# Optimization experiments

Measured on AMD Instinct MI355X. Metric: run time of the kernel, lower is better.

The kernel has to match this reference:

```python
import jax, jax.numpy as jnp
import numpy as np

# ---------------- irreps metadata: list of (mul, l, parity) ----------------
IR_A  = [(1, 0, 1)]                                        # '0e' input scalars
IR_B  = [(10,0,1),(10,0,-1),(10,0,1),(5,1,1),(5,1,-1)]     # Gate input, dim 60
IR_C  = [(10,0,1),(10,0,-1),(5,1,1),(5,1,-1)]              # Gate output, dim 50
IR_D  = [(1,0,-1),(6,0,1)]                                 # '0o + 6x0e', dim 7
IR_SH = [(1,0,1),(1,1,-1)]                                 # '0e + 1o'
CONVS = [(IR_A,IR_B),(IR_C,IR_B),(IR_C,IR_B),(IR_C,IR_B),(IR_C,IR_D)]
R_BASIS  = 2
DIAMETER = 5.0   # source used 1.5 -> degenerate 1^3 kernel; enlarged to exercise the steerable conv
STEP     = 1.0

def irdim(ir):
    return sum(m*(2*l+1) for m,l,_ in ir)

def irslices(ir):
    out, o = [], 0
    for m,l,_ in ir:
        d = m*(2*l+1); out.append(slice(o,o+d)); o += d
    return out

# normalized Clebsch-Gordan (wigner3j * sqrt(2*l_out+1)) for l<=1
_eps = np.zeros((3,3,3))
for a,b,c in [(0,1,2),(1,2,0),(2,0,1)]:
    _eps[a,b,c] = 1.0; _eps[b,a,c] = -1.0
CG = {
    (0,0,0): np.ones((1,1,1)),
    (0,1,1): np.eye(3).reshape(1,3,3),
    (1,0,1): np.eye(3).reshape(3,1,3),
    (1,1,0): (np.eye(3)/np.sqrt(3.0)).reshape(3,3,1),
    (1,1,1): _eps/np.sqrt(2.0),
}

def tp_ins(ir1, iro):
    ins = []
    for i1,(m1,l1,p1) in enumerate(ir1):
        for i2,(m2,l2,p2) in enumerate(IR_SH):
            for io,(mo,lo,po) in enumerate(iro):
                if po == p1*p2 and abs(l1-l2) <= lo <= l1+l2:
                    ins.append((i1,i2,io))
    return ins

def tp_numel(ir1, iro):
    return sum(R_BASIS*ir1[i1][0]*IR_SH[i2][0]*iro[io][0] for i1,i2,io in tp_ins(ir1,iro))

def lin_ins(ir1, iro):
    return [(i,j) for i,(m1,l1,p1) in enumerate(ir1)
                  for j,(m2,l2,p2) in enumerate(iro) if l1==l2 and p1==p2]

def lin_numel(ir1, iro):
    return sum(ir1[i][0]*iro[j][0] for i,j in lin_ins(ir1,iro))

def _lattice_features():
    # lattice offsets, smooth_finite radial basis (with cutoff) and SH ('0e+1o', component norm)
    r = DIAMETER/2.0
    s = int(np.floor(r/STEP))
    c = np.arange(-s, s+1, dtype=np.float64)*STEP
    lat = np.stack(np.meshgrid(c, c, c, indexing='ij'), -1)            # [K,K,K,3]
    d = np.linalg.norm(lat, axis=-1)
    vals = np.linspace(0.0, r, R_BASIS+2)[1:-1]
    step = vals[1]-vals[0]
    diff = (d[...,None]-vals)/step
    sus = lambda t: np.where(t>0, np.exp(-1.0/np.where(t>0, t, 1.0)), 0.0)
    emb = 1.14136*np.exp(2.0)*sus(diff+1.0)*sus(1.0-diff)              # [K,K,K,R]
    unit = lat/np.maximum(d, 1e-9)[...,None]
    sh = np.concatenate([np.ones_like(d)[...,None],
                         np.sqrt(3.0)*unit[...,[1,2,0]]], -1)          # [K,K,K,4], e3nn (y,z,x) order
    return jnp.asarray(emb, jnp.float32), jnp.asarray(sh, jnp.float32)

EMB, SH = _lattice_features()

def build_kernel(ir_in, ir_out, tw, lw):
    sin, sout, ssh = irslices(ir_in), irslices(ir_out), irslices(IR_SH)
    K = EMB.shape[0]
    k = jnp.zeros((K, K, K, irdim(ir_in), irdim(ir_out)), jnp.float32)
    off = 0
    for i1,i2,io in tp_ins(ir_in, ir_out):
        m1,l1,_ = ir_in[i1]; m2,l2,_ = IR_SH[i2]; mo,lo,_ = ir_out[io]
        n = R_BASIS*m1*m2*mo
        w = tw[off:off+n].reshape(R_BASIS, m1, mo); off += n           # m2 == 1 for SH
        cg = jnp.asarray(CG[(l1,l2,lo)], jnp.float32)
        alpha = 1.0/np.sqrt(m1*m2*R_BASIS)
        shseg = SH[..., ssh[i2]]                                       # [K,K,K,2l2+1]
        blk = alpha*jnp.einsum('xyzr,ruw,xyzj,ijk->xyzuiwk', EMB, w, shseg, cg)
        k = k.at[:,:,:, sin[i1], sout[io]].add(
            blk.reshape(K, K, K, m1*(2*l1+1), mo*(2*lo+1)))
    # self-connection Linear at the kernel center (radial basis vanishes at r=0)
    M = jnp.zeros((irdim(ir_in), irdim(ir_out)), jnp.float32)
    off = 0
    for i,j in lin_ins(ir_in, ir_out):
        m1,l1,_ = ir_in[i]; mo,_,_ = ir_out[j]
        w = lw[off:off+m1*mo].reshape(m1, mo); off += m1*mo
        eye = jnp.eye(2*l1+1, dtype=jnp.float32)
        blk = (1.0/np.sqrt(m1))*jnp.einsum('uw,ik->uiwk', w, eye)
        M = M.at[sin[i], sout[j]].add(blk.reshape(m1*(2*l1+1), mo*(2*l1+1)))
    cc = K//2
    return k.at[cc, cc, cc].set(M)

def equiv_conv(x, k):
    return jax.lax.conv_general_dilated(x, k, (1,1,1), 'SAME',
        dimension_numbers=('NXYZC', 'XYZIO', 'NXYZC'))

def gate(y):
    # Gate('10x0e+10x0o', [gelu, tanh], '10x0e', [sigmoid], '5x1e+5x1o')
    s = jnp.concatenate([jax.nn.gelu(y[..., :10]), jnp.tanh(y[..., 10:20])], -1)
    g = jax.nn.sigmoid(y[..., 20:30])                                  # 10 gate scalars
    v = y[..., 30:60].reshape(y.shape[:-1]+(10,3))*g[..., None]        # gate 5x1e + 5x1o
    return jnp.concatenate([s, v.reshape(y.shape[:-1]+(30,))], -1)

def _forward(x, tws, lws):
    y = x
    for i,(a,b) in enumerate(CONVS):
        y = equiv_conv(y, build_kernel(a, b, tws[i], lws[i]))
        if i < len(CONVS)-1:
            y = gate(y)
    return jnp.sum(y, axis=(1, 2, 3))                                  # [B, 7]

def setup_inputs() -> dict:
    key = jax.random.key(0)
    ks = jax.random.split(key, 11)
    inp = {'x': jax.random.normal(ks[0], (2, 48, 48, 48, 1), jnp.float32)}
    for i,(a,b) in enumerate(CONVS):
        inp[f'tp_w{i}'] = jax.random.normal(ks[1+i], (tp_numel(a,b),), jnp.float32)
        inp[f'lin_w{i}'] = jax.random.normal(ks[6+i], (lin_numel(a,b),), jnp.float32)
    return inp

def reference(x, tp_w0, tp_w1, tp_w2, tp_w3, tp_w4,
              lin_w0, lin_w1, lin_w2, lin_w3, lin_w4):
    return _forward(x, [tp_w0, tp_w1, tp_w2, tp_w3, tp_w4],
                    [lin_w0, lin_w1, lin_w2, lin_w3, lin_w4])
```

## Files before the change

### kernel.cpp

```cpp
#include <hip/hip_runtime.h>
#include <hip/hip_bf16.h>
#include <math.h>


typedef __attribute__((ext_vector_type(8))) short bf16x8;
typedef __attribute__((ext_vector_type(4))) float f32x4;
typedef __attribute__((ext_vector_type(4))) unsigned int u32x4;

struct TpPath { int off, ci, co, m1, l1, i2, mo, lo; float alpha; };
struct LinPath { int off, ci, co, m1, l, mo; float norm; };

__device__ __constant__ TpPath g_tp[19] = {
  {0,  0,  0, 1, 0, 0, 10, 0, 0.70710678f},
  {20, 0, 20, 1, 0, 0, 10, 0, 0.70710678f},
  {40, 0, 45, 1, 0, 1,  5, 1, 0.70710678f},
  {0,    0,  0, 10, 0, 0, 10, 0, 0.22360680f},
  {200,  0, 20, 10, 0, 0, 10, 0, 0.22360680f},
  {400,  0, 45, 10, 0, 1,  5, 1, 0.22360680f},
  {500, 10, 10, 10, 0, 0, 10, 0, 0.22360680f},
  {700, 10, 30, 10, 0, 1,  5, 1, 0.22360680f},
  {800, 20, 30,  5, 1, 0,  5, 1, 0.31622777f},
  {850, 20, 10,  5, 1, 1, 10, 0, 0.31622777f},
  {950, 20, 45,  5, 1, 1,  5, 1, 0.31622777f},
  {1000,35, 45,  5, 1, 0,  5, 1, 0.31622777f},
  {1050,35,  0,  5, 1, 1, 10, 0, 0.31622777f},
  {1150,35, 20,  5, 1, 1, 10, 0, 0.31622777f},
  {1250,35, 30,  5, 1, 1,  5, 1, 0.31622777f},
  {0,    0, 1, 10, 0, 0, 6, 0, 0.22360680f},
  {120, 10, 0, 10, 0, 0, 1, 0, 0.22360680f},
  {140, 20, 0,  5, 1, 1, 1, 0, 0.31622777f},
  {150, 35, 1,  5, 1, 1, 6, 0, 0.31622777f},
};

__device__ __constant__ LinPath g_lin[9] = {
  {0,  0,  0, 1, 0, 10, 1.0f},
  {10, 0, 20, 1, 0, 10, 1.0f},
  {0,   0,  0, 10, 0, 10, 0.31622777f},
  {100, 0, 20, 10, 0, 10, 0.31622777f},
  {200,10, 10, 10, 0, 10, 0.31622777f},
  {300,20, 30,  5, 1,  5, 0.44721360f},
  {325,35, 45,  5, 1,  5, 0.44721360f},
  {0,  0, 1, 10, 0, 6, 0.31622777f},
  {60,10, 0, 10, 0, 1, 0.31622777f},
};

__device__ inline float sus_f(float t) { return t > 0.f ? __expf(-1.f / t) : 0.f; }

__global__ void build_tp_kernel(const float* __restrict__ tw, float* __restrict__ kbuf,
                                int CIN, int COUT, int path_base) {
  TpPath p = g_tp[path_base + blockIdx.x];
  const int dl1 = 2 * p.l1 + 1, dlo = 2 * p.lo + 1;
  const int du = p.m1 * dl1, dw = p.mo * dlo;
  const int total = 125 * du * dw;
  const float C0 = 1.14136f * expf(2.0f);
  for (int e = threadIdx.x; e < total; e += blockDim.x) {
    int xyz = e / (du * dw);
    int rem = e % (du * dw);
    int ui = rem / dw, wk = rem % dw;
    int u = ui / dl1, i = ui % dl1;
    int w = wk / dlo, kk = wk % dlo;
    int kx = xyz / 25, ky = (xyz / 5) % 5, kz = xyz % 5;
    float cx = (float)(kx - 2), cy = (float)(ky - 2), cz = (float)(kz - 2);
    float d = sqrtf(cx * cx + cy * cy + cz * cz);
    float t = 1.2f * d;
    float e0 = C0 * sus_f(t) * sus_f(2.f - t);
    float e1 = C0 * sus_f(t - 1.f) * sus_f(3.f - t);
    float radial = e0 * tw[p.off + (0 * p.m1 + u) * p.mo + w] +
                   e1 * tw[p.off + (1 * p.m1 + u) * p.mo + w];
    float invd = (d > 0.f) ? 1.f / d : 0.f;
    const float s3 = 1.7320508f;
    float sh1[3] = { s3 * cy * invd, s3 * cz * invd, s3 * cx * invd };
    float shfac;
    if (p.l1 == 0 && p.i2 == 0)      shfac = 1.f;
    else if (p.l1 == 0)              shfac = sh1[kk];
    else if (p.i2 == 0)              shfac = (i == kk) ? 1.f : 0.f;
    else if (p.lo == 0)              shfac = sh1[i] * 0.57735027f;
    else {
      if (i == kk) shfac = 0.f;
      else {
        int j = 3 - i - kk;
        float sgn = (j == (i + 1) % 3) ? 1.f : -1.f;
        shfac = sgn * sh1[j] * 0.70710678f;
      }
    }
    kbuf[(size_t)(xyz * CIN + p.ci + ui) * COUT + p.co + wk] = p.alpha * radial * shfac;
  }
}

__global__ void set_center_kernel(const float* __restrict__ lw, float* __restrict__ kbuf,
                                  int CIN, int COUT, int lin_base, int nlin) {
  for (int l = 0; l < nlin; l++) {
    LinPath q = g_lin[lin_base + l];
    int dl = 2 * q.l + 1;
    int tot = q.m1 * q.mo * dl;
    for (int e = threadIdx.x; e < tot; e += blockDim.x) {
      int u = e / (q.mo * dl);
      int r = e % (q.mo * dl);
      int w = r / dl, ii = r % dl;
      kbuf[(size_t)(62 * CIN + q.ci + u * dl + ii) * COUT + q.co + w * dl + ii] =
          q.norm * lw[q.off + u * q.mo + w];
    }
  }
}

__global__ void convert_w(const float* __restrict__ kbuf, unsigned short* __restrict__ kwbT,
                          int CIN, int COUT) {
  int idx = blockIdx.x * 256 + threadIdx.x;
  if (idx >= 125 * 64 * 64) return;
  int tap = idx >> 12, co = (idx >> 6) & 63, ci = idx & 63;
  float v = (ci < CIN && co < COUT) ? kbuf[((size_t)tap * CIN + ci) * COUT + co] : 0.f;
  __hip_bfloat16 h = __float2bfloat16(v);
  kwbT[idx] = *(unsigned short*)&h;
}

__global__ void build_w0(const float* __restrict__ k0, unsigned short* __restrict__ wb0L) {
  int idx = blockIdx.x * 256 + threadIdx.x;
  if (idx >= 5 * 2 * 64 * 32) return;
  int k = idx & 31, co = (idx >> 5) & 63, mf = (idx >> 11) & 1, dxi = idx >> 12;
  float v = 0.f;
  if (co < 60) {
    if (mf == 0) {
      int dy = k >> 3, dz = k & 7;
      if (dz < 5) v = k0[(size_t)(((dxi * 5 + dy) * 5 + dz)) * 60 + co];
    } else {
      int kg = k >> 3, dz = k & 7;
      if (kg == 0 && dz < 5) v = k0[(size_t)(((dxi * 5 + 4) * 5 + dz)) * 60 + co];
    }
  }
  __hip_bfloat16 h = __float2bfloat16(v);
  wb0L[idx] = *(unsigned short*)&h;
}

__device__ inline float gelu_f(float x) {
  float inner = 0.79788456f * (x + 0.044715f * x * x * x);
  return 0.5f * x * (1.f + tanhf(inner));
}
__device__ inline float sigm_f(float x) { return 1.f / (1.f + __expf(-x)); }

__device__ inline int eidx(int c, int z) {
  return c * 16 + ((((z >> 2) ^ (c & 3)) << 2) | (z & 3));
}
__device__ inline int oidx(int z, int p) { return z * 32 + (p ^ z); }
__device__ inline int uidx(int e) {
  return (e & ~31) | ((e & 31) ^ ((e >> 5) & 15));
}

__device__ inline void gate_tile(const float* my, unsigned int* myO, int z) {
#pragma unroll
  for (int p = 0; p < 25; p++) {
    float a0, a1;
    if (p < 5) {
      a0 = gelu_f(my[eidx(2 * p, z)]);
      a1 = gelu_f(my[eidx(2 * p + 1, z)]);
    } else if (p < 10) {
      a0 = tanhf(my[eidx(2 * p, z)]);
      a1 = tanhf(my[eidx(2 * p + 1, z)]);
    } else {
      int q0 = 2 * (p - 10), q1 = q0 + 1;
      a0 = my[eidx(30 + q0, z)] * sigm_f(my[eidx(20 + q0 / 3, z)]);
      a1 = my[eidx(30 + q1, z)] * sigm_f(my[eidx(20 + q1 / 3, z)]);
    }
    __hip_bfloat162 p2;
    p2.x = __float2bfloat16(a0);
    p2.y = __float2bfloat16(a1);
    myO[oidx(z, p)] = *(unsigned int*)&p2;
  }
#pragma unroll
  for (int p = 25; p < 32; p++) myO[oidx(z, p)] = 0u;
}

template <int NT>
__device__ inline void epilogue_gate(f32x4 (&acc)[3][NT], float* my,
                                     unsigned short* out_, int n, int x, int y,
                                     int l, int lm, int kg) {
  unsigned int* myO = (unsigned int*)(my + 1024);
#pragma unroll
  for (int zt = 0; zt < 3; zt++) {
#pragma unroll
    for (int nt = 0; nt < NT; nt++)
      *(f32x4*)(my + (lm + 16 * nt) * 16 + ((kg ^ (lm & 3)) << 2)) = acc[zt][nt];
    if (l < 16) gate_tile(my, myO, l);
    unsigned int* gout = (unsigned int*)out_ +
        ((size_t)(((n * 48 + x) * 48 + y) * 48 + 16 * zt)) * 32;
#pragma unroll 1
    for (int e = l; e < 512; e += 64) gout[e] = myO[uidx(e)];
  }
}

template <int CIN, int COUT, int MODE>
__global__ __launch_bounds__(768, 3)
void conv_mfma(const unsigned short* __restrict__ act, const short* __restrict__ kwbT,
               const unsigned short* __restrict__ zguard, void* __restrict__ out_) {
  constexpr int NTH = (MODE == 0) ? 2 : 1;
  constexpr int KC = (CIN + 31) / 32;
  __shared__ __align__(16) unsigned int Albs[16 * 48 * 32];

  const int tid = threadIdx.x;
  const int l = tid & 63;
  const int w = tid >> 6;
  const int wp = (MODE == 0) ? (w % 6) : w;
  const int ch = (MODE == 0) ? (w / 6) : 0;
  const int lm = l & 15;
  const int kg = l >> 4;
  const int co_off = ch * 32;

  const int bid = blockIdx.x;
  const int yb = bid % 4;
  const int x = (bid / 4) % 48;
  const int n = bid / (4 * 48);

  int g_off[8]; bool g_ok[8];
#pragma unroll
  for (int i = 0; i < 8; i++) {
    int e = tid + i * 768;
    int yi = e / 384;
    int rem = e % 384;
    int zin = rem >> 3, u = rem & 7;
    int usrc = u ^ (zin & 7);
    int yin = 12 * yb + yi - 2;
    g_ok[i] = (yin >= 0) && (yin < 48);
    int yc = min(max(yin, 0), 47);
    g_off[i] = (yc * 48 + zin) * 64 + usrc * 8;
  }

  f32x4 acc[2][3][NTH];
#pragma unroll
  for (int yy = 0; yy < 2; yy++)
#pragma unroll
    for (int zt = 0; zt < 3; zt++)
#pragma unroll
      for (int nt = 0; nt < NTH; nt++) acc[yy][zt][nt] = (f32x4){0.f, 0.f, 0.f, 0.f};

  const int xlo = max(x - 2, 0), xhi = min(x + 2, 47);

#pragma unroll 1
  for (int xin = xlo; xin <= xhi; ++xin) {
    __syncthreads();
    const unsigned short* pb = act + (size_t)((n * 48 + xin) * 2304) * 64;
#pragma unroll
    for (int i = 0; i < 8; i++) {
      const unsigned short* src = g_ok[i] ? (pb + g_off[i]) : zguard;
      __builtin_amdgcn_global_load_lds(
          (const __attribute__((address_space(1))) unsigned int*)src,
          (__attribute__((address_space(3))) unsigned int*)(Albs + (size_t)(i * 768 + w * 64) * 4),
          16, 0, 0);
    }
    __syncthreads();

    if (MODE == 0 || w < 6) {
      const int dxi = xin - x + 2;
      const short* Albs_s = (const short*)Albs;
#pragma unroll 1
      for (int dy = 0; dy < 5; dy++) {
        const int tapbase = (dxi * 5 + dy) * 5;
#pragma unroll
        for (int dz = 0; dz < 5; dz++) {
          bf16x8 bfr[NTH * KC];
          {
            const short* wb_ = kwbT + ((size_t)(tapbase + dz) << 12) +
                               (co_off + lm) * 64 + kg * 8;
#pragma unroll
            for (int nt = 0; nt < NTH; nt++)
#pragma unroll
              for (int kc = 0; kc < KC; kc++)
                bfr[nt * KC + kc] = *(const bf16x8*)(wb_ + nt * 1024 + kc * 32);
          }
          bf16x8 afr[2][3][KC];
#pragma unroll
          for (int zt = 0; zt < 3; zt++) {
            const int zraw = 16 * zt + lm + dz - 2;
            const int zc = min(max(zraw, 0), 47);
            const bool zval = (zraw >= 0) && (zraw < 48);
#pragma unroll
            for (int yy = 0; yy < 2; yy++) {
              const int yrow = 2 * wp + yy + dy;
              const int rowoff = (yrow * 48 + zc) * 64;
#pragma unroll
              for (int kc = 0; kc < KC; kc++) {
                int u = (4 * kc + kg) ^ (zc & 7);
                bf16x8 v = *(const bf16x8*)(Albs_s + rowoff + u * 8);
                afr[yy][zt][kc] = zval ? v : (bf16x8)(short)0;
              }
            }
          }
#pragma unroll
          for (int yy = 0; yy < 2; yy++)
#pragma unroll
            for (int zt = 0; zt < 3; zt++)
#pragma unroll
              for (int nt = 0; nt < NTH; nt++)
#pragma unroll
                for (int kc = 0; kc < KC; kc++)
                  acc[yy][zt][nt] = __builtin_amdgcn_mfma_f32_16x16x32_bf16(
                      afr[yy][zt][kc], bfr[nt * KC + kc], acc[yy][zt][nt], 0, 0, 0);
        }
      }
    }
  }

  if constexpr (MODE == 0) {
    __syncthreads();
    float* base = (float*)Albs;
    int par = 0;
#pragma unroll
    for (int yy = 0; yy < 2; yy++) {
#pragma unroll
      for (int zt = 0; zt < 3; zt++) {
        float* my = base + par * 9216 + wp * 1536;
        unsigned int* myO = (unsigned int*)(my + 1024);
#pragma unroll
        for (int nt = 0; nt < NTH; nt++)
          *(f32x4*)(my + (co_off + lm + 16 * nt) * 16 + ((kg ^ (lm & 3)) << 2)) =
              acc[yy][zt][nt];
        __syncthreads();
        if (ch == 0 && l < 16) gate_tile(my, myO, l);
        __syncthreads();
        unsigned int* gout = (unsigned int*)out_ +
            ((size_t)(((n * 48 + x) * 48 + (12 * yb + 2 * wp + yy)) * 48 + 16 * zt)) * 32;
#pragma unroll
        for (int q = 0; q < 4; q++) {
          int e = ch * 256 + q * 64 + l;
          gout[e] = myO[uidx(e)];
        }
        par ^= 1;
      }
    }
  } else {
    if (w < 6) {
      float s = 0.f;
#pragma unroll
      for (int yy = 0; yy < 2; yy++)
#pragma unroll
        for (int zt = 0; zt < 3; zt++)
#pragma unroll
          for (int r = 0; r < 4; r++) s += acc[yy][zt][0][r];
      s += __shfl_xor(s, 16);
      s += __shfl_xor(s, 32);
      if (l < 7) atomicAdd(&((float*)out_)[n * 7 + l], s);
    }
  }
}

__global__ __launch_bounds__(256, 4)
void conv0_mfma(const float* __restrict__ in_, const short* __restrict__ wb0L,
                unsigned short* __restrict__ out_) {
  __shared__ float A0[8 * 72];
  __shared__ __align__(16) float outbuf0[4 * 1536];

  const int tid = threadIdx.x;
  const int l = tid & 63;
  const int w = tid >> 6;
  const int lm = l & 15;
  const int kg = l >> 4;
  const int yb = blockIdx.x % 12;
  const int x = (blockIdx.x / 12) % 48;
  const int n = blockIdx.x / (12 * 48);

  f32x4 acc[3][4];
#pragma unroll
  for (int zt = 0; zt < 3; zt++)
#pragma unroll
    for (int nt = 0; nt < 4; nt++) acc[zt][nt] = (f32x4){0.f, 0.f, 0.f, 0.f};

  for (int dxi = 0; dxi < 5; dxi++) {
    int xin = x + dxi - 2;
    if (xin < 0 || xin >= 48) continue;
    __syncthreads();
    for (int e = tid; e < 8 * 72; e += 256) {
      int yi = e / 72, zz = e % 72;
      int yin = 4 * yb + yi - 2, zin = zz - 2;
      A0[e] = (yin >= 0 && yin < 48 && zin >= 0 && zin < 48)
                  ? in_[(size_t)((n * 48 + xin) * 48 + yin) * 48 + zin] : 0.f;
    }
    __syncthreads();
#pragma unroll
    for (int mf = 0; mf < 2; mf++) {
      const short* wbp = wb0L + ((size_t)(dxi * 2 + mf) * 64 + lm) * 32 + kg * 8;
      bf16x8 bfr[4];
#pragma unroll
      for (int nt = 0; nt < 4; nt++) bfr[nt] = *(const bf16x8*)(wbp + nt * 16 * 32);
      const int row = mf ? (w + 4) : (w + kg);
#pragma unroll
      for (int zt = 0; zt < 3; zt++) {
        const float* ap = A0 + row * 72 + 16 * zt + lm;
        union { bf16x8 v; unsigned short s[8]; } af;
#pragma unroll
        for (int j = 0; j < 8; j++) {
          __hip_bfloat16 h = __float2bfloat16(ap[j]);
          af.s[j] = *(unsigned short*)&h;
        }
#pragma unroll
        for (int nt = 0; nt < 4; nt++)
          acc[zt][nt] = __builtin_amdgcn_mfma_f32_16x16x32_bf16(
              af.v, bfr[nt], acc[zt][nt], 0, 0, 0);
      }
    }
  }

  float* my = outbuf0 + w * 1536;
  epilogue_gate<4>(acc, my, out_, n, x, 4 * yb + w, l, lm, kg);
}

__global__ void sum_z(const unsigned short* __restrict__ act, float* __restrict__ zs) {
  int gw = blockIdx.x * 4 + (threadIdx.x >> 6);
  int ci = threadIdx.x & 63;
  const unsigned short* p = act + (size_t)gw * 48 * 64 + ci;
  float tot = 0.f, s0 = 0.f, s1 = 0.f, s46 = 0.f, s47 = 0.f;
#pragma unroll 4
  for (int z = 0; z < 48; z++) {
    unsigned short h = p[z * 64];
    float v = __bfloat162float(*(__hip_bfloat16*)&h);
    tot += v;
    if (z == 0) s0 = v;
    if (z == 1) s1 = v;
    if (z == 46) s46 = v;
    if (z == 47) s47 = v;
  }
  float* o = zs + (size_t)gw * 320 + ci;
  o[0]   = tot - s46 - s47;
  o[64]  = tot - s47;
  o[128] = tot;
  o[192] = tot - s0;
  o[256] = tot - s0 - s1;
}

__global__ void sum_y(const float* __restrict__ zs, float* __restrict__ ys) {
  int idx = blockIdx.x * 256 + threadIdx.x;
  if (idx >= 153600) return;
  int ci = idx & 63;
  int r = idx >> 6;
  int rz = r % 5;
  int r2 = r / 5;
  int ry = r2 % 5;
  int nx = r2 / 5;
  int y0 = max(0, ry - 2), y1 = min(47, 45 + ry);
  float s = 0.f;
  const float* p = zs + (size_t)(nx * 48) * 320 + rz * 64 + ci;
  for (int y = y0; y <= y1; y++) s += p[(size_t)y * 320];
  ys[((size_t)nx * 25 + ry * 5 + rz) * 64 + ci] = s;
}

__global__ void sum_x(const float* __restrict__ ys, float* __restrict__ xs) {
  int idx = blockIdx.x * 256 + threadIdx.x;
  if (idx >= 16000) return;
  int ci = idx & 63;
  int r = idx >> 6;
  int tap = r % 125;
  int n = r / 125;
  int rx = tap / 25, ry = (tap / 5) % 5, rz = tap % 5;
  int x0 = max(0, rx - 2), x1 = min(47, 45 + rx);
  float s = 0.f;
  const float* p = ys + (size_t)(n * 48) * 1600 + (ry * 5 + rz) * 64 + ci;
  for (int xx = x0; xx <= x1; xx++) s += p[(size_t)xx * 1600];
  xs[(size_t)n * 8000 + tap * 64 + ci] = s;
}

__global__ void contract4(const float* __restrict__ k4, const float* __restrict__ xs,
                          float* __restrict__ out) {
  int t = threadIdx.x;
  int pair = t & 15, chunk = t >> 4;
  if (pair >= 14) return;
  int n = pair / 7, co = pair % 7;
  int t0 = chunk * 8, t1 = min(t0 + 8, 125);
  float s = 0.f;
  for (int tap = t0; tap < t1; tap++)
    for (int ci = 0; ci < 50; ci++)
      s += k4[((size_t)tap * 50 + ci) * 7 + co] * xs[(size_t)n * 8000 + tap * 64 + ci];
  atomicAdd(&out[n * 7 + co], s);
}

extern "C" void kernel_launch(void* const* d_in, const int* in_sizes, int n_in,
                              void* d_out, int out_size, void* d_ws, size_t ws_size,
                              hipStream_t stream) {
  const float* x   = (const float*)d_in[0];
  const float* tw0 = (const float*)d_in[1];
  const float* lw0 = (const float*)d_in[2];
  const float* tw1 = (const float*)d_in[3];
  const float* lw1 = (const float*)d_in[4];
  const float* tw2 = (const float*)d_in[5];
  const float* lw2 = (const float*)d_in[6];
  const float* tw3 = (const float*)d_in[7];
  const float* lw3 = (const float*)d_in[8];
  const float* tw4 = (const float*)d_in[9];
  const float* lw4 = (const float*)d_in[10];

  float* ws = (float*)d_ws;
  float* k0 = ws;
  float* k1 = k0 + 7500;
  float* k2 = k1 + 375000;
  float* k3 = k2 + 375000;
  float* k4 = k3 + 375000;
  unsigned short* actA = (unsigned short*)(ws + 1200000);
  unsigned short* actB = actA + 14155776;
  unsigned short* wb1 = (unsigned short*)(ws + 15360000);
  unsigned short* wb2 = wb1 + 512000;
  unsigned short* wb3 = wb2 + 512000;
  unsigned short* wb0L = wb3 + 512000;
  unsigned short* zg   = wb0L + 20480;
  float* zs = (float*)actA;
  float* ys = k1;
  float* xs = k2;

  hipMemsetAsync(ws, 0, (size_t)1176250 * sizeof(float), stream);
  hipMemsetAsync(zg, 0, 64, stream);
  hipMemsetAsync(d_out, 0, (size_t)out_size * sizeof(float), stream);

  build_tp_kernel<<<3, 128, 0, stream>>>(tw0, k0, 1, 60, 0);
  build_tp_kernel<<<12, 128, 0, stream>>>(tw1, k1, 50, 60, 3);
  build_tp_kernel<<<12, 128, 0, stream>>>(tw2, k2, 50, 60, 3);
  build_tp_kernel<<<12, 128, 0, stream>>>(tw3, k3, 50, 60, 3);
  build_tp_kernel<<<4, 128, 0, stream>>>(tw4, k4, 50, 7, 15);
  set_center_kernel<<<1, 256, 0, stream>>>(lw0, k0, 1, 60, 0, 2);
  set_center_kernel<<<1, 256, 0, stream>>>(lw1, k1, 50, 60, 2, 5);
  set_center_kernel<<<1, 256, 0, stream>>>(lw2, k2, 50, 60, 2, 5);
  set_center_kernel<<<1, 256, 0, stream>>>(lw3, k3, 50, 60, 2, 5);
  set_center_kernel<<<1, 256, 0, stream>>>(lw4, k4, 50, 7, 7, 2);

  convert_w<<<2000, 256, 0, stream>>>(k1, wb1, 50, 60);
  convert_w<<<2000, 256, 0, stream>>>(k2, wb2, 50, 60);
  convert_w<<<2000, 256, 0, stream>>>(k3, wb3, 50, 60);
  build_w0<<<80, 256, 0, stream>>>(k0, wb0L);

  const int grid0 = 2 * 48 * 12;
  const int grid  = 2 * 48 * 4;
  conv0_mfma<<<grid0, 256, 0, stream>>>(x, (const short*)wb0L, actA);
  conv_mfma<50, 60, 0><<<grid, 768, 0, stream>>>(actA, (const short*)wb1, zg, actB);
  conv_mfma<50, 60, 0><<<grid, 768, 0, stream>>>(actB, (const short*)wb2, zg, actA);
  conv_mfma<50, 60, 0><<<grid, 768, 0, stream>>>(actA, (const short*)wb3, zg, actB);
  sum_z<<<1152, 256, 0, stream>>>(actB, zs);
  sum_y<<<600, 256, 0, stream>>>(zs, ys);
  sum_x<<<63, 256, 0, stream>>>(ys, xs);
  contract4<<<1, 256, 0, stream>>>(k4, xs, (float*)d_out);
}
```

Before: 1.861 ms.

## Restructure middle conv kernel to 16 waves with one y-row per wave

```diff
diff --git a/kernel.cpp b/kernel.cpp
--- a/kernel.cpp
+++ b/kernel.cpp
@@ -187,49 +187,47 @@
   }
 }
 
-template <int CIN, int COUT, int MODE>
-__global__ __launch_bounds__(768, 3)
-void conv_mfma(const unsigned short* __restrict__ act, const short* __restrict__ kwbT,
-               const unsigned short* __restrict__ zguard, void* __restrict__ out_) {
-  constexpr int NTH = (MODE == 0) ? 2 : 1;
+template <int CIN, int COUT>
+__global__ __launch_bounds__(1024, 4)
+void conv_mfma16(const unsigned short* __restrict__ act, const short* __restrict__ kwbT,
+                 const unsigned short* __restrict__ zguard, void* __restrict__ out_) {
+  constexpr int NTH = 2;
   constexpr int KC = (CIN + 31) / 32;
-  __shared__ __align__(16) unsigned int Albs[16 * 48 * 32];
+  __shared__ __align__(16) unsigned int Albs[24576];
 
   const int tid = threadIdx.x;
   const int l = tid & 63;
   const int w = tid >> 6;
-  const int wp = (MODE == 0) ? (w % 6) : w;
-  const int ch = (MODE == 0) ? (w / 6) : 0;
+  const int wp = w & 7;
+  const int ch = w >> 3;
   const int lm = l & 15;
   const int kg = l >> 4;
   const int co_off = ch * 32;
 
   const int bid = blockIdx.x;
-  const int yb = bid % 4;
-  const int x = (bid / 4) % 48;
-  const int n = bid / (4 * 48);
-
-  int g_off[8]; bool g_ok[8];
-#pragma unroll
-  for (int i = 0; i < 8; i++) {
-    int e = tid + i * 768;
+  const int yb = bid % 6;
+  const int x = (bid / 6) % 48;
+  const int n = bid / (6 * 48);
+
+  int g_off[5]; bool g_ok[5];
+#pragma unroll
+  for (int i = 0; i < 5; i++) {
+    int e = tid + i * 1024;
     int yi = e / 384;
     int rem = e % 384;
     int zin = rem >> 3, u = rem & 7;
     int usrc = u ^ (zin & 7);
-    int yin = 12 * yb + yi - 2;
-    g_ok[i] = (yin >= 0) && (yin < 48);
+    int yin = 8 * yb + yi - 2;
+    g_ok[i] = (e < 4608) && (yin >= 0) && (yin < 48);
     int yc = min(max(yin, 0), 47);
-    g_off[i] = (yc * 48 + zin) * 64 + usrc * 8;
-  }
-
-  f32x4 acc[2][3][NTH];
-#pragma unroll
-  for (int yy = 0; yy < 2; yy++)
-#pragma unroll
-    for (int zt = 0; zt < 3; zt++)
-#pragma unroll
-      for (int nt = 0; nt < NTH; nt++) acc[yy][zt][nt] = (f32x4){0.f, 0.f, 0.f, 0.f};
+    g_off[i] = (min(yc, 47) * 48 + zin) * 64 + usrc * 8;
+  }
+
+  f32x4 acc[3][NTH];
+#pragma unroll
+  for (int zt = 0; zt < 3; zt++)
+#pragma unroll
+    for (int nt = 0; nt < NTH; nt++) acc[zt][nt] = (f32x4){0.f, 0.f, 0.f, 0.f};
 
   const int xlo = max(x - 2, 0), xhi = min(x + 2, 47);
 
@@ -238,106 +236,82 @@
     __syncthreads();
     const unsigned short* pb = act + (size_t)((n * 48 + xin) * 2304) * 64;
 #pragma unroll
-    for (int i = 0; i < 8; i++) {
+    for (int i = 0; i < 5; i++) {
       const unsigned short* src = g_ok[i] ? (pb + g_off[i]) : zguard;
       __builtin_amdgcn_global_load_lds(
           (const __attribute__((address_space(1))) unsigned int*)src,
-          (__attribute__((address_space(3))) unsigned int*)(Albs + (size_t)(i * 768 + w * 64) * 4),
+          (__attribute__((address_space(3))) unsigned int*)(Albs + (size_t)(tid + i * 1024) * 4),
           16, 0, 0);
     }
     __syncthreads();
 
-    if (MODE == 0 || w < 6) {
-      const int dxi = xin - x + 2;
-      const short* Albs_s = (const short*)Albs;
+    const int dxi = xin - x + 2;
+    const short* Albs_s = (const short*)Albs;
 #pragma unroll 1
-      for (int dy = 0; dy < 5; dy++) {
-        const int tapbase = (dxi * 5 + dy) * 5;
-#pragma unroll
-        for (int dz = 0; dz < 5; dz++) {
-          bf16x8 bfr[NTH * KC];
-          {
-            const short* wb_ = kwbT + ((size_t)(tapbase + dz) << 12) +
-                               (co_off + lm) * 64 + kg * 8;
-#pragma unroll
-            for (int nt = 0; nt < NTH; nt++)
-#pragma unroll
-              for (int kc = 0; kc < KC; kc++)
-                bfr[nt * KC + kc] = *(const bf16x8*)(wb_ + nt * 1024 + kc * 32);
+    for (int dy = 0; dy < 5; dy++) {
+      const int yrow = wp + dy;
+      const int tapbase = (dxi * 5 + dy) * 5;
+#pragma unroll
+      for (int dz = 0; dz < 5; dz++) {
+        bf16x8 bfr[NTH * KC];
+        {
+          const short* wb_ = kwbT + ((size_t)(tapbase + dz) << 12) +
+                             (co_off + lm) * 64 + kg * 8;
+#pragma unroll
+          for (int nt = 0; nt < NTH; nt++)
+#pragma unroll
+            for (int kc = 0; kc < KC; kc++)
+              bfr[nt * KC + kc] = *(const bf16x8*)(wb_ + nt * 1024 + kc * 32);
+        }
+        bf16x8 afr[3][KC];
+#pragma unroll
+        for (int zt = 0; zt < 3; zt++) {
+          const int zraw = 16 * zt + lm + dz - 2;
+          const int zc = min(max(zraw, 0), 47);
+          const bool zval = (zraw >= 0) && (zraw < 48);
+          const int rowoff = (yrow * 48 + zc) * 64;
+#pragma unroll
+          for (int kc = 0; kc < KC; kc++) {
+            int u = (4 * kc + kg) ^ (zc & 7);
+            bf16x8 v = *(const bf16x8*)(Albs_s + rowoff + u * 8);
+            afr[zt][kc] = zval ? v : (bf16x8)(short)0;
           }
-          bf16x8 afr[2][3][KC];
-#pragma unroll
-          for (int zt = 0; zt < 3; zt++) {
-            const int zraw = 16 * zt + lm + dz - 2;
-            const int zc = min(max(zraw, 0), 47);
-            const bool zval = (zraw >= 0) && (zraw < 48);
-#pragma unroll
-            for (int yy = 0; yy < 2; yy++) {
-              const int yrow = 2 * wp + yy + dy;
-              const int rowoff = (yrow * 48 + zc) * 64;
-#pragma unroll
-              for (int kc = 0; kc < KC; kc++) {
-                int u = (4 * kc + kg) ^ (zc & 7);
-                bf16x8 v = *(const bf16x8*)(Albs_s + rowoff + u * 8);
-                afr[yy][zt][kc] = zval ? v : (bf16x8)(short)0;
-              }
-            }
-          }
-#pragma unroll
-          for (int yy = 0; yy < 2; yy++)
-#pragma unroll
-            for (int zt = 0; zt < 3; zt++)
-#pragma unroll
-              for (int nt = 0; nt < NTH; nt++)
-#pragma unroll
-                for (int kc = 0; kc < KC; kc++)
-                  acc[yy][zt][nt] = __builtin_amdgcn_mfma_f32_16x16x32_bf16(
-                      afr[yy][zt][kc], bfr[nt * KC + kc], acc[yy][zt][nt], 0, 0, 0);
         }
+#pragma unroll
+        for (int zt = 0; zt < 3; zt++)
+#pragma unroll
+          for (int nt = 0; nt < NTH; nt++)
+#pragma unroll
+            for (int kc = 0; kc < KC; kc++)
+              acc[zt][nt] = __builtin_amdgcn_mfma_f32_16x16x32_bf16(
+                  afr[zt][kc], bfr[nt * KC + kc], acc[zt][nt], 0, 0, 0);
       }
     }
   }
 
-  if constexpr (MODE == 0) {
+  __syncthreads();
+  float* base = (float*)Albs;
+  const int y = 8 * yb + wp;
+  int par = 0;
+#pragma unroll
+  for (int zt = 0; zt < 3; zt++) {
+    float* my = base + par * 12288 + wp * 1536;
+    unsigned int* myO = (unsigned int*)(my + 1024);
+#pragma unroll
+    for (int nt = 0; nt < NTH; nt++)
+      *(f32x4*)(my + (co_off + lm + 16 * nt) * 16 + ((kg ^ (lm & 3)) << 2)) =
+          acc[zt][nt];
     __syncthreads();
-    float* base = (float*)Albs;
-    int par = 0;
-#pragma unroll
-    for (int yy = 0; yy < 2; yy++) {
-#pragma unroll
-      for (int zt = 0; zt < 3; zt++) {
-        float* my = base + par * 9216 + wp * 1536;
-        unsigned int* myO = (unsigned int*)(my + 1024);
-#pragma unroll
-        for (int nt = 0; nt < NTH; nt++)
-          *(f32x4*)(my + (co_off + lm + 16 * nt) * 16 + ((kg ^ (lm & 3)) << 2)) =
-              acc[yy][zt][nt];
-        __syncthreads();
-        if (ch == 0 && l < 16) gate_tile(my, myO, l);
-        __syncthreads();
-        unsigned int* gout = (unsigned int*)out_ +
-            ((size_t)(((n * 48 + x) * 48 + (12 * yb + 2 * wp + yy)) * 48 + 16 * zt)) * 32;
-#pragma unroll
-        for (int q = 0; q < 4; q++) {
-          int e = ch * 256 + q * 64 + l;
-          gout[e] = myO[uidx(e)];
-        }
-        par ^= 1;
-      }
-    }
-  } else {
-    if (w < 6) {
-      float s = 0.f;
-#pragma unroll
-      for (int yy = 0; yy < 2; yy++)
-#pragma unroll
-        for (int zt = 0; zt < 3; zt++)
-#pragma unroll
-          for (int r = 0; r < 4; r++) s += acc[yy][zt][0][r];
-      s += __shfl_xor(s, 16);
-      s += __shfl_xor(s, 32);
-      if (l < 7) atomicAdd(&((float*)out_)[n * 7 + l], s);
-    }
+    if (ch == 0 && l < 16) gate_tile(my, myO, l);
+    __syncthreads();
+    unsigned int* gout = (unsigned int*)out_ +
+        ((size_t)(((n * 48 + x) * 48 + y) * 48 + 16 * zt)) * 32;
+#pragma unroll
+    for (int q = 0; q < 4; q++) {
+      int e = ch * 256 + q * 64 + l;
+      gout[e] = myO[uidx(e)];
+    }
+    par ^= 1;
   }
 }
 
@@ -522,11 +496,11 @@
   build_w0<<<80, 256, 0, stream>>>(k0, wb0L);
 
   const int grid0 = 2 * 48 * 12;
-  const int grid  = 2 * 48 * 4;
+  const int grid  = 2 * 48 * 6;
   conv0_mfma<<<grid0, 256, 0, stream>>>(x, (const short*)wb0L, actA);
-  conv_mfma<50, 60, 0><<<grid, 768, 0, stream>>>(actA, (const short*)wb1, zg, actB);
-  conv_mfma<50, 60, 0><<<grid, 768, 0, stream>>>(actB, (const short*)wb2, zg, actA);
-  conv_mfma<50, 60, 0><<<grid, 768, 0, stream>>>(actA, (const short*)wb3, zg, actB);
+  conv_mfma16<50, 60><<<grid, 1024, 0, stream>>>(actA, (const short*)wb1, zg, actB);
+  conv_mfma16<50, 60><<<grid, 1024, 0, stream>>>(actB, (const short*)wb2, zg, actA);
+  conv_mfma16<50, 60><<<grid, 1024, 0, stream>>>(actA, (const short*)wb3, zg, actB);
   sum_z<<<1152, 256, 0, stream>>>(actB, zs);
   sum_y<<<600, 256, 0, stream>>>(zs, ys);
   sum_x<<<63, 256, 0, stream>>>(ys, xs);
```

Measured after the change: 2.860 ms. +53.7%, slower.
